# Performance work log

Hardware: AMD Instinct MI355X
Metric: run time of the kernel (lower is better)

Reference implementation:

```python
import jax, jax.numpy as jnp
import numpy as np

# Network dimensions (match init_kwargs)
N_IN, N_HID, N_OUT = 2048, 8192, 1024
N = N_IN + N_HID + N_OUT
BATCH = 512


def setup_inputs() -> dict:
    key = jax.random.key(0)
    k_w, k_b, k_x = jax.random.split(key, 3)
    # GraphNet._init_connections: Xavier-ish std based on (n_inputs + n_outputs)
    std = (2.0 / (N_IN + N_OUT)) ** 0.5
    W = jax.random.normal(k_w, (N, N), dtype=jnp.float32) * std
    # mask: inputs -> hidden, hidden -> outputs (fixed 3-level DAG)
    mask = jnp.zeros((N, N), dtype=jnp.float32)
    mask = mask.at[:N_IN, N_IN:N_IN + N_HID].set(1.0)
    mask = mask.at[N_IN:N_IN + N_HID, N_IN + N_HID:].set(1.0)
    # bias is zero-init in the module; use small random values so it is exercised
    bias = jax.random.normal(k_b, (N,), dtype=jnp.float32) * 0.01
    x = jax.random.normal(k_x, (BATCH, N_IN), dtype=jnp.float32)
    return {"x": x, "W": W, "bias": bias, "mask": mask}


def reference(x, W, bias, mask):
    # Faithful translation of GraphNet.forward for the canonical 3-level
    # topology produced by _init_connections/_compute_levels:
    #   level 0: input nodes [0, N_IN)
    #   level 1: hidden nodes [N_IN, N_IN+N_HID)  -> ReLU
    #   level 2: output nodes [N_IN+N_HID, N)     -> identity (OUTPUT type)
    W_eff = W * mask                       # [N, N] masked adjacency
    B = x.shape[0]
    h = jnp.zeros((B, N), dtype=x.dtype).at[:, :N_IN].set(x)
    # level 1 (hidden): pre_act = h @ W_eff[:, idx] + bias[idx]; ReLU
    pre_h = h @ W_eff[:, N_IN:N_IN + N_HID] + bias[N_IN:N_IN + N_HID]
    h = h.at[:, N_IN:N_IN + N_HID].set(jax.nn.relu(pre_h))
    # level 2 (outputs): pre-activation only (node_type == OUTPUT -> no ReLU)
    pre_o = h @ W_eff[:, N_IN + N_HID:] + bias[N_IN + N_HID:]
    return pre_o                            # h[:, output_indices]
```

## Files before the change

### kernel.cpp

```cpp
#include <hip/hip_runtime.h>

#define N_IN 2048
#define N_HID 8192
#define N_OUT 1024
#define NTOT 11264

typedef __attribute__((ext_vector_type(4))) float f32x4;
typedef __attribute__((ext_vector_type(4))) short short4v;
typedef __attribute__((ext_vector_type(8))) short short8v;
typedef __attribute__((ext_vector_type(2))) unsigned u32x2;

__device__ inline short f2bf(float f) {
    unsigned u = __float_as_uint(f);
    return (short)((u + 0x7fffu + ((u >> 16) & 1u)) >> 16);
}

__device__ inline float bf2f(short s) {
    return __uint_as_float(((unsigned)(unsigned short)s) << 16);
}

__device__ inline unsigned cvt_pk_bf16(float lo, float hi) {
    unsigned r;
    asm("v_cvt_pk_bf16_f32 %0, %1, %2" : "=v"(r) : "v"(lo), "v"(hi));
    return r;
}

__device__ inline int perm64(int c) {
    return (c & 32) + (((c >> 2) & 3) << 3) + (((c >> 4) & 1) << 2) + (c & 3);
}

__device__ inline void gload_lds16(const void* g, void* l) {
    __builtin_amdgcn_global_load_lds(
        (const __attribute__((address_space(1))) unsigned int*)g,
        (__attribute__((address_space(3))) unsigned int*)l, 16, 0, 0);
}

#define WAITV(N) { asm volatile("s_waitcnt vmcnt(" #N ")" ::: "memory"); \
                   __builtin_amdgcn_sched_barrier(0); }
#define BARRIER  { asm volatile("s_waitcnt lgkmcnt(0)" ::: "memory"); \
                   __builtin_amdgcn_sched_barrier(0); \
                   __builtin_amdgcn_s_barrier(); \
                   __builtin_amdgcn_sched_barrier(0); }

__global__ __launch_bounds__(512, 2) void gemm1(
    const float* __restrict__ x,
    const float* __restrict__ W,
    const float* __restrict__ bias,
    short* __restrict__ hOut)
{
    __shared__ __align__(16) short As[2][128 * 64];
    __shared__ __align__(16) short Bs[2][128][72];

    const int bid = blockIdx.x;
    const int xcd = bid & 7;
    const int j   = bid >> 3;
    const int bx  = xcd * 8 + (j >> 2);
    const int by  = j & 3;

    const int t    = threadIdx.x;
    const int lane = t & 63;
    const int wid  = t >> 6;
    const int wr   = wid >> 2;
    const int wc   = wid & 3;
    const int brow = by * 128;
    const int bcol = bx * 128;
    const int l15  = lane & 15;
    const int lg   = lane >> 4;

    const int ar = t >> 2;
    const int kq = (t & 3) * 16;
    const int pbase = ((kq & 32) + ((kq >> 4) & 1) * 4) * 2;
    const int arx = (ar & 7) << 4;
    const float* xrow = x + (size_t)(brow + ar) * N_IN + kq;

    const int nb   = (lane & 7) + 8 * (wid >> 1);
    const int kblk = ((lane >> 3) & 7) + 8 * (wid & 1);
    const int n0 = nb * 4, k0 = kblk * 4;
    const int p0 = perm64(k0);

    f32x4 acc[4][2] = {};
    f32x4 bv0[4], bv1[4], bv2[4];
    f32x4 av0[4], av1[4];

    const float* wp0 = &W[(size_t)k0 * NTOT + (N_IN + bcol + n0)];

#define B_LOAD(TT, BV) { \
    const float* wp = wp0 + (size_t)(TT) * 64 * NTOT; \
    _Pragma("unroll") for (int jj = 0; jj < 4; ++jj) \
        BV[jj] = *reinterpret_cast<const f32x4*>(wp + (size_t)jj * NTOT); }

#define A_LOADR(TT, AV) { \
    const float* xp = xrow + (TT) * 64; \
    _Pragma("unroll") for (int jj = 0; jj < 4; ++jj) \
        AV[jj] = *reinterpret_cast<const f32x4*>(xp + jj * 4); }

#define A_WRITE(TT, AV) { \
    char* dst = (char*)As + ((TT) & 1) * 16384; \
    _Pragma("unroll") for (int jj = 0; jj < 4; ++jj) { \
        u32x2 s; \
        s[0] = cvt_pk_bf16(AV[jj][0], AV[jj][1]); \
        s[1] = cvt_pk_bf16(AV[jj][2], AV[jj][3]); \
        *reinterpret_cast<u32x2*>( \
            dst + ((ar * 128 + pbase + jj * 16) ^ arx)) = s; } }

#define B_WRITE(TT, BV) { \
    short* bsb = &Bs[(TT) & 1][0][0]; \
    _Pragma("unroll") for (int i = 0; i < 4; ++i) { \
        u32x2 s; \
        s[0] = cvt_pk_bf16(BV[0][i], BV[1][i]); \
        s[1] = cvt_pk_bf16(BV[2][i], BV[3][i]); \
        *reinterpret_cast<u32x2*>(bsb + (n0 + i) * 72 + p0) = s; } }

#define COMPUTE(TT) { \
    const char*  ab = (const char*)As + ((TT) & 1) * 16384; \
    const short* bb = &Bs[(TT) & 1][0][0]; \
    short8v a[2][4], b[2][2]; \
    _Pragma("unroll") for (int g = 0; g < 2; ++g) { \
        const int koff = g * 64 + lg * 16; \
        _Pragma("unroll") for (int m = 0; m < 4; ++m) { \
            const int r = wr * 64 + m * 16 + l15; \
            a[g][m] = *reinterpret_cast<const short8v*>( \
                ab + ((r * 128 + koff) ^ ((r & 7) << 4))); } \
        _Pragma("unroll") for (int n = 0; n < 2; ++n) { \
            const int r = wc * 32 + n * 16 + l15; \
            b[g][n] = *reinterpret_cast<const short8v*>( \
                (const char*)(bb + r * 72) + koff); } } \
    __builtin_amdgcn_s_setprio(1); \
    _Pragma("unroll") for (int g = 0; g < 2; ++g) \
      _Pragma("unroll") for (int m = 0; m < 4; ++m) \
        _Pragma("unroll") for (int n = 0; n < 2; ++n) \
            acc[m][n] = __builtin_amdgcn_mfma_f32_16x16x32_bf16( \
                a[g][m], b[g][n], acc[m][n], 0, 0, 0); \
    __builtin_amdgcn_s_setprio(0); }

#define ITER(T, BVL, AVL, AVW, BVW) { \
    B_LOAD(T + 3, BVL); \
    A_LOADR(T + 2, AVL); \
    WAITV(8); \
    A_WRITE(T + 1, AVW); \
    B_WRITE(T + 1, BVW); \
    COMPUTE(T); \
    BARRIER; }

    B_LOAD(0, bv0);
    A_LOADR(0, av0);
    B_LOAD(1, bv1);
    A_LOADR(1, av1);
    B_LOAD(2, bv2);
    WAITV(12);
    A_WRITE(0, av0);
    B_WRITE(0, bv0);
    BARRIER;

    for (int tt = 0; tt < 24; tt += 6) {
        ITER(tt,     bv0, av0, av1, bv1);
        ITER(tt + 1, bv1, av1, av0, bv2);
        ITER(tt + 2, bv2, av0, av1, bv0);
        ITER(tt + 3, bv0, av1, av0, bv1);
        ITER(tt + 4, bv1, av0, av1, bv2);
        ITER(tt + 5, bv2, av1, av0, bv0);
    }
    ITER(24, bv0, av0, av1, bv1);
    ITER(25, bv1, av1, av0, bv2);
    ITER(26, bv2, av0, av1, bv0);
    ITER(27, bv0, av1, av0, bv1);
    ITER(28, bv1, av0, av1, bv2);

    A_LOADR(31, av1);
    WAITV(4);
    A_WRITE(30, av0);
    B_WRITE(30, bv0);
    COMPUTE(29);
    BARRIER;
    WAITV(0);
    A_WRITE(31, av1);
    B_WRITE(31, bv1);
    COMPUTE(30);
    BARRIER;
    COMPUTE(31);

#undef B_LOAD
#undef A_LOADR
#undef A_WRITE
#undef B_WRITE
#undef COMPUTE
#undef ITER

#pragma unroll
    for (int m = 0; m < 4; ++m) {
        const int row0 = brow + wr * 64 + m * 16 + lg * 4;
#pragma unroll
        for (int n = 0; n < 2; ++n) {
            const int col  = bcol + wc * 32 + n * 16 + l15;
            const int pcol = (col & ~63) + perm64(col & 63);
            const float bb = bias[N_IN + col];
#pragma unroll
            for (int q = 0; q < 4; ++q) {
                float v = acc[m][n][q] + bb;
                v = v > 0.f ? v : 0.f;
                hOut[(size_t)(row0 + q) * N_HID + pcol] = f2bf(v);
            }
        }
    }
}

__global__ __launch_bounds__(512, 2) void gemm2(
    const short* __restrict__ A,
    const float* __restrict__ W,
    short* __restrict__ pOut)
{
    __shared__ __align__(16) short As[4][128 * 64];
    __shared__ __align__(16) short Bs[2][128][72];

    const int bid = blockIdx.x;
    const int xcd = bid & 7;
    const int j   = bid >> 3;
    const int xz  = xcd * 8 + (j >> 2);
    const int bx  = xz & 7;
    const int bz  = xz >> 3;
    const int by  = j & 3;

    const int t    = threadIdx.x;
    const int lane = t & 63;
    const int wid  = t >> 6;
    const int wr   = wid >> 2;
    const int wc   = wid & 3;
    const int brow = by * 128;
    const int bcol = bx * 128;
    const int l15  = lane & 15;
    const int lg   = lane >> 4;
    const int ks   = bz * 1024;

    const int arow = lane >> 3;
    const int asw  = ((lane & 7) * 16) ^ (arow << 4);

    const int nb   = (lane & 7) + 8 * (wid >> 1);
    const int kblk = ((lane >> 3) & 7) + 8 * (wid & 1);
    const int n0 = nb * 4, k0 = kblk * 4;
    const int p0 = perm64(k0);

    const char*  Abytes = (const char*)A;
    const size_t lda_b  = (size_t)N_HID * 2;

    f32x4 acc[4][2] = {};
    f32x4 bv0[4], bv1[4], bv2[4], bv3[4];

    const float* wp0 = &W[(size_t)(N_IN + ks + k0) * NTOT
                          + (N_IN + N_HID + bcol + n0)];

#define B_LOAD(TT, BV) { \
    const float* wp = wp0 + (size_t)(TT) * 64 * NTOT; \
    _Pragma("unroll") for (int jj = 0; jj < 4; ++jj) \
        BV[jj] = *reinterpret_cast<const f32x4*>(wp + (size_t)jj * NTOT); }

#define A_LOAD(TT) { \
    char* dst = (char*)As + ((TT) & 3) * 16384; \
    _Pragma("unroll") for (int i = 0; i < 2; ++i) { \
        const int c = wid * 2 + i; \
        gload_lds16(Abytes + (size_t)(brow + c * 8 + arow) * lda_b \
                          + (size_t)(ks + (TT) * 64) * 2 + asw, \
                    dst + c * 1024); } }

#define B_WRITE(TT, BV) { \
    short* bsb = &Bs[(TT) & 1][0][0]; \
    _Pragma("unroll") for (int i = 0; i < 4; ++i) { \
        u32x2 s; \
        s[0] = cvt_pk_bf16(BV[0][i], BV[1][i]); \
        s[1] = cvt_pk_bf16(BV[2][i], BV[3][i]); \
        *reinterpret_cast<u32x2*>(bsb + (n0 + i) * 72 + p0) = s; } }

#define COMPUTE(TT) { \
    const char*  ab = (const char*)As + ((TT) & 3) * 16384; \
    const short* bb = &Bs[(TT) & 1][0][0]; \
    short8v a[2][4], b[2][2]; \
    _Pragma("unroll") for (int g = 0; g < 2; ++g) { \
        const int koff = g * 64 + lg * 16; \
        _Pragma("unroll") for (int m = 0; m < 4; ++m) { \
            const int r = wr * 64 + m * 16 + l15; \
            a[g][m] = *reinterpret_cast<const short8v*>( \
                ab + ((r * 128 + koff) ^ ((r & 7) << 4))); } \
        _Pragma("unroll") for (int n = 0; n < 2; ++n) { \
            const int r = wc * 32 + n * 16 + l15; \
            b[g][n] = *reinterpret_cast<const short8v*>( \
                (const char*)(bb + r * 72) + koff); } } \
    __builtin_amdgcn_s_setprio(1); \
    _Pragma("unroll") for (int g = 0; g < 2; ++g) \
      _Pragma("unroll") for (int m = 0; m < 4; ++m) \
        _Pragma("unroll") for (int n = 0; n < 2; ++n) \
            acc[m][n] = __builtin_amdgcn_mfma_f32_16x16x32_bf16( \
                a[g][m], b[g][n], acc[m][n], 0, 0, 0); \
    __builtin_amdgcn_s_setprio(0); }

#define ITER(T, BVL, BVW) { \
    B_LOAD(T + 3, BVL); A_LOAD(T + 3); \
    WAITV(12); \
    B_WRITE(T + 1, BVW); \
    COMPUTE(T); \
    BARRIER; }

    B_LOAD(0, bv0); A_LOAD(0);
    B_LOAD(1, bv1); A_LOAD(1);
    B_LOAD(2, bv2); A_LOAD(2);
    WAITV(12);
    B_WRITE(0, bv0);
    BARRIER;

    const int nt = 16;
    for (int tt = 0; tt + 4 < nt; tt += 4) {
        ITER(tt,     bv3, bv1);
        ITER(tt + 1, bv0, bv2);
        ITER(tt + 2, bv1, bv3);
        ITER(tt + 3, bv2, bv0);
    }
    ITER(nt - 4, bv3, bv1);

    WAITV(6);
    B_WRITE(nt - 2, bv2);
    COMPUTE(nt - 3);
    BARRIER;
    WAITV(0);
    B_WRITE(nt - 1, bv3);
    COMPUTE(nt - 2);
    BARRIER;
    COMPUTE(nt - 1);

#undef B_LOAD
#undef A_LOAD
#undef B_WRITE
#undef COMPUTE
#undef ITER

    short* po = pOut + (size_t)bz * (512 * N_OUT);
#pragma unroll
    for (int m = 0; m < 4; ++m) {
        const int row0 = brow + wr * 64 + m * 16 + lg * 4;
#pragma unroll
        for (int n = 0; n < 2; ++n) {
            const int col = bcol + wc * 32 + n * 16 + l15;
#pragma unroll
            for (int q = 0; q < 4; ++q)
                po[(size_t)(row0 + q) * N_OUT + col] = f2bf(acc[m][n][q]);
        }
    }
}

__global__ __launch_bounds__(256) void reduce_bias(
    const short* __restrict__ part,
    const float* __restrict__ bias,
    float* __restrict__ out)
{
    const int idx = (blockIdx.x * 256 + threadIdx.x) * 4;
    f32x4 s = *reinterpret_cast<const f32x4*>(&bias[N_IN + N_HID + (idx & 1023)]);
#pragma unroll
    for (int sp = 0; sp < 8; ++sp) {
        const short4v p = *reinterpret_cast<const short4v*>(
            &part[(size_t)sp * 524288 + idx]);
#pragma unroll
        for (int jj = 0; jj < 4; ++jj) s[jj] += bf2f(p[jj]);
    }
    *reinterpret_cast<f32x4*>(&out[idx]) = s;
}

extern "C" void kernel_launch(void* const* d_in, const int* in_sizes, int n_in,
                              void* d_out, int out_size, void* d_ws, size_t ws_size,
                              hipStream_t stream) {
    const float* x    = (const float*)d_in[0];
    const float* W    = (const float*)d_in[1];
    const float* bias = (const float*)d_in[2];
    float* out = (float*)d_out;

    short* h    = (short*)d_ws;
    short* part = (short*)((char*)d_ws + (size_t)(8 << 20));

    gemm1<<<dim3(256), dim3(512), 0, stream>>>(x, W, bias, h);

    gemm2<<<dim3(256), dim3(512), 0, stream>>>(h, W, part);

    reduce_bias<<<dim3(512), dim3(256), 0, stream>>>(part, bias, out);
}
```

Before: 59.32 us.

## Fuse both GEMMs and reduction into one persistent kernel with atomic counters

Merges gemm1, gemm2 and reduce_bias into one kernel of 256 blocks. A block's GEMM2 tile waits on per-tile atomic counters for the GEMM1 tiles it depends on. The last block finishing each output tile does the split-K reduction plus bias. This removes two kernel launch gaps and lets GEMM2 tiles start before all of GEMM1 completes. The cost is a memset launch, spin-waiting on counters, and reliance on all 256 blocks being co-resident to avoid deadlock.

```diff
diff --git a/kernel.cpp b/kernel.cpp
--- a/kernel.cpp
+++ b/kernel.cpp
@@ -14,21 +14,17 @@
     unsigned u = __float_as_uint(f);
     return (short)((u + 0x7fffu + ((u >> 16) & 1u)) >> 16);
 }
-
 __device__ inline float bf2f(short s) {
     return __uint_as_float(((unsigned)(unsigned short)s) << 16);
 }
-
 __device__ inline unsigned cvt_pk_bf16(float lo, float hi) {
     unsigned r;
     asm("v_cvt_pk_bf16_f32 %0, %1, %2" : "=v"(r) : "v"(lo), "v"(hi));
     return r;
 }
-
 __device__ inline int perm64(int c) {
     return (c & 32) + (((c >> 2) & 3) << 3) + (((c >> 4) & 1) << 2) + (c & 3);
 }
-
 __device__ inline void gload_lds16(const void* g, void* l) {
     __builtin_amdgcn_global_load_lds(
         (const __attribute__((address_space(1))) unsigned int*)g,
@@ -42,47 +38,57 @@
                    __builtin_amdgcn_s_barrier(); \
                    __builtin_amdgcn_sched_barrier(0); }
 
-__global__ __launch_bounds__(512, 2) void gemm1(
+__global__ __launch_bounds__(512, 2) void fused_net(
     const float* __restrict__ x,
     const float* __restrict__ W,
     const float* __restrict__ bias,
-    short* __restrict__ hOut)
+    short* __restrict__ h,
+    short* __restrict__ part,
+    float* __restrict__ out,
+    int* __restrict__ cnt)
 {
-    __shared__ __align__(16) short As[2][128 * 64];
-    __shared__ __align__(16) short Bs[2][128][72];
+    __shared__ __align__(16) char smem[102400];
+    __shared__ int isFin;
 
     const int bid = blockIdx.x;
-    const int xcd = bid & 7;
-    const int j   = bid >> 3;
-    const int bx  = xcd * 8 + (j >> 2);
-    const int by  = j & 3;
-
     const int t    = threadIdx.x;
     const int lane = t & 63;
     const int wid  = t >> 6;
     const int wr   = wid >> 2;
     const int wc   = wid & 3;
-    const int brow = by * 128;
-    const int bcol = bx * 128;
     const int l15  = lane & 15;
     const int lg   = lane >> 4;
 
-    const int ar = t >> 2;
-    const int kq = (t & 3) * 16;
-    const int pbase = ((kq & 32) + ((kq >> 4) & 1) * 4) * 2;
-    const int arx = (ar & 7) << 4;
-    const float* xrow = x + (size_t)(brow + ar) * N_IN + kq;
-
-    const int nb   = (lane & 7) + 8 * (wid >> 1);
-    const int kblk = ((lane >> 3) & 7) + 8 * (wid & 1);
-    const int n0 = nb * 4, k0 = kblk * 4;
-    const int p0 = perm64(k0);
-
-    f32x4 acc[4][2] = {};
-    f32x4 bv0[4], bv1[4], bv2[4];
-    f32x4 av0[4], av1[4];
-
-    const float* wp0 = &W[(size_t)k0 * NTOT + (N_IN + bcol + n0)];
+    int* cnt1 = cnt;
+    int* cnt2 = cnt + 32;
+
+    {
+        char*  As1 = smem;
+        short* Bs1 = (short*)(smem + 32768);
+
+        const int xcd = bid & 7;
+        const int j   = bid >> 3;
+        const int bx  = xcd * 8 + (j >> 2);
+        const int by  = j & 3;
+        const int brow = by * 128;
+        const int bcol = bx * 128;
+
+        const int ar = t >> 2;
+        const int kq = (t & 3) * 16;
+        const int pbase = ((kq & 32) + ((kq >> 4) & 1) * 4) * 2;
+        const int arx = (ar & 7) << 4;
+        const float* xrow = x + (size_t)(brow + ar) * N_IN + kq;
+
+        const int nb   = (lane & 7) + 8 * (wid >> 1);
+        const int kblk = ((lane >> 3) & 7) + 8 * (wid & 1);
+        const int n0 = nb * 4, k0 = kblk * 4;
+        const int p0 = perm64(k0);
+
+        f32x4 acc[4][2] = {};
+        f32x4 bv0[4], bv1[4], bv2[4];
+        f32x4 av0[4], av1[4];
+
+        const float* wp0 = &W[(size_t)k0 * NTOT + (N_IN + bcol + n0)];
 
 #define B_LOAD(TT, BV) { \
     const float* wp = wp0 + (size_t)(TT) * 64 * NTOT; \
@@ -95,7 +101,7 @@
         AV[jj] = *reinterpret_cast<const f32x4*>(xp + jj * 4); }
 
 #define A_WRITE(TT, AV) { \
-    char* dst = (char*)As + ((TT) & 1) * 16384; \
+    char* dst = As1 + ((TT) & 1) * 16384; \
     _Pragma("unroll") for (int jj = 0; jj < 4; ++jj) { \
         u32x2 s; \
         s[0] = cvt_pk_bf16(AV[jj][0], AV[jj][1]); \
@@ -104,7 +110,7 @@
             dst + ((ar * 128 + pbase + jj * 16) ^ arx)) = s; } }
 
 #define B_WRITE(TT, BV) { \
-    short* bsb = &Bs[(TT) & 1][0][0]; \
+    short* bsb = Bs1 + ((TT) & 1) * (128 * 72); \
     _Pragma("unroll") for (int i = 0; i < 4; ++i) { \
         u32x2 s; \
         s[0] = cvt_pk_bf16(BV[0][i], BV[1][i]); \
@@ -112,8 +118,8 @@
         *reinterpret_cast<u32x2*>(bsb + (n0 + i) * 72 + p0) = s; } }
 
 #define COMPUTE(TT) { \
-    const char*  ab = (const char*)As + ((TT) & 1) * 16384; \
-    const short* bb = &Bs[(TT) & 1][0][0]; \
+    const char*  ab = As1 + ((TT) & 1) * 16384; \
+    const short* bb = Bs1 + ((TT) & 1) * (128 * 72); \
     short8v a[2][4], b[2][2]; \
     _Pragma("unroll") for (int g = 0; g < 2; ++g) { \
         const int koff = g * 64 + lg * 16; \
@@ -142,42 +148,42 @@
     COMPUTE(T); \
     BARRIER; }
 
-    B_LOAD(0, bv0);
-    A_LOADR(0, av0);
-    B_LOAD(1, bv1);
-    A_LOADR(1, av1);
-    B_LOAD(2, bv2);
-    WAITV(12);
-    A_WRITE(0, av0);
-    B_WRITE(0, bv0);
-    BARRIER;
-
-    for (int tt = 0; tt < 24; tt += 6) {
-        ITER(tt,     bv0, av0, av1, bv1);
-        ITER(tt + 1, bv1, av1, av0, bv2);
-        ITER(tt + 2, bv2, av0, av1, bv0);
-        ITER(tt + 3, bv0, av1, av0, bv1);
-        ITER(tt + 4, bv1, av0, av1, bv2);
-        ITER(tt + 5, bv2, av1, av0, bv0);
-    }
-    ITER(24, bv0, av0, av1, bv1);
-    ITER(25, bv1, av1, av0, bv2);
-    ITER(26, bv2, av0, av1, bv0);
-    ITER(27, bv0, av1, av0, bv1);
-    ITER(28, bv1, av0, av1, bv2);
-
-    A_LOADR(31, av1);
-    WAITV(4);
-    A_WRITE(30, av0);
-    B_WRITE(30, bv0);
-    COMPUTE(29);
-    BARRIER;
-    WAITV(0);
-    A_WRITE(31, av1);
-    B_WRITE(31, bv1);
-    COMPUTE(30);
-    BARRIER;
-    COMPUTE(31);
+        B_LOAD(0, bv0);
+        A_LOADR(0, av0);
+        B_LOAD(1, bv1);
+        A_LOADR(1, av1);
+        B_LOAD(2, bv2);
+        WAITV(12);
+        A_WRITE(0, av0);
+        B_WRITE(0, bv0);
+        BARRIER;
+
+        for (int tt = 0; tt < 24; tt += 6) {
+            ITER(tt,     bv0, av0, av1, bv1);
+            ITER(tt + 1, bv1, av1, av0, bv2);
+            ITER(tt + 2, bv2, av0, av1, bv0);
+            ITER(tt + 3, bv0, av1, av0, bv1);
+            ITER(tt + 4, bv1, av0, av1, bv2);
+            ITER(tt + 5, bv2, av1, av0, bv0);
+        }
+        ITER(24, bv0, av0, av1, bv1);
+        ITER(25, bv1, av1, av0, bv2);
+        ITER(26, bv2, av0, av1, bv0);
+        ITER(27, bv0, av1, av0, bv1);
+        ITER(28, bv1, av0, av1, bv2);
+
+        A_LOADR(31, av1);
+        WAITV(4);
+        A_WRITE(30, av0);
+        B_WRITE(30, bv0);
+        COMPUTE(29);
+        BARRIER;
+        WAITV(0);
+        A_WRITE(31, av1);
+        B_WRITE(31, bv1);
+        COMPUTE(30);
+        BARRIER;
+        COMPUTE(31);
 
 #undef B_LOAD
 #undef A_LOADR
@@ -187,66 +193,73 @@
 #undef ITER
 
 #pragma unroll
-    for (int m = 0; m < 4; ++m) {
-        const int row0 = brow + wr * 64 + m * 16 + lg * 4;
-#pragma unroll
-        for (int n = 0; n < 2; ++n) {
-            const int col  = bcol + wc * 32 + n * 16 + l15;
-            const int pcol = (col & ~63) + perm64(col & 63);
-            const float bb = bias[N_IN + col];
-#pragma unroll
-            for (int q = 0; q < 4; ++q) {
-                float v = acc[m][n][q] + bb;
-                v = v > 0.f ? v : 0.f;
-                hOut[(size_t)(row0 + q) * N_HID + pcol] = f2bf(v);
+        for (int m = 0; m < 4; ++m) {
+            const int row0 = brow + wr * 64 + m * 16 + lg * 4;
+#pragma unroll
+            for (int n = 0; n < 2; ++n) {
+                const int col  = bcol + wc * 32 + n * 16 + l15;
+                const int pcol = (col & ~63) + perm64(col & 63);
+                const float bb = bias[N_IN + col];
+#pragma unroll
+                for (int q = 0; q < 4; ++q) {
+                    float v = acc[m][n][q] + bb;
+                    v = v > 0.f ? v : 0.f;
+                    h[(size_t)(row0 + q) * N_HID + pcol] = f2bf(v);
+                }
             }
         }
+
+        asm volatile("s_waitcnt vmcnt(0)" ::: "memory");
+        __syncthreads();
+        if (t == 0)
+            __hip_atomic_fetch_add(&cnt1[(bx >> 3) * 4 + by], 1,
+                                   __ATOMIC_RELEASE, __HIP_MEMORY_SCOPE_AGENT);
     }
-}
-
-__global__ __launch_bounds__(512, 2) void gemm2(
-    const short* __restrict__ A,
-    const float* __restrict__ W,
-    short* __restrict__ pOut)
-{
-    __shared__ __align__(16) short As[4][128 * 64];
-    __shared__ __align__(16) short Bs[2][128][72];
-
-    const int bid = blockIdx.x;
-    const int xcd = bid & 7;
-    const int j   = bid >> 3;
-    const int xz  = xcd * 8 + (j >> 2);
-    const int bx  = xz & 7;
-    const int bz  = xz >> 3;
-    const int by  = j & 3;
-
-    const int t    = threadIdx.x;
-    const int lane = t & 63;
-    const int wid  = t >> 6;
-    const int wr   = wid >> 2;
-    const int wc   = wid & 3;
-    const int brow = by * 128;
-    const int bcol = bx * 128;
-    const int l15  = lane & 15;
-    const int lg   = lane >> 4;
-    const int ks   = bz * 1024;
-
-    const int arow = lane >> 3;
-    const int asw  = ((lane & 7) * 16) ^ (arow << 4);
-
-    const int nb   = (lane & 7) + 8 * (wid >> 1);
-    const int kblk = ((lane >> 3) & 7) + 8 * (wid & 1);
-    const int n0 = nb * 4, k0 = kblk * 4;
-    const int p0 = perm64(k0);
-
-    const char*  Abytes = (const char*)A;
-    const size_t lda_b  = (size_t)N_HID * 2;
-
-    f32x4 acc[4][2] = {};
-    f32x4 bv0[4], bv1[4], bv2[4], bv3[4];
-
-    const float* wp0 = &W[(size_t)(N_IN + ks + k0) * NTOT
-                          + (N_IN + N_HID + bcol + n0)];
+
+    int fx, fy;
+    {
+        char*  As2 = smem;
+        short* Bs2 = (short*)(smem + 65536);
+
+        const int xcd = bid & 7;
+        const int j   = bid >> 3;
+        const int xz  = xcd * 8 + (j >> 2);
+        const int bx2 = xz & 7;
+        const int bz  = xz >> 3;
+        const int by2 = j & 3;
+        fx = bx2; fy = by2;
+        const int brow = by2 * 128;
+        const int bcol = bx2 * 128;
+        const int ks   = bz * 1024;
+
+        {
+            const int slot = bz * 4 + by2;
+            if (t == 0) {
+                while (__hip_atomic_load(&cnt1[slot], __ATOMIC_RELAXED,
+                                         __HIP_MEMORY_SCOPE_AGENT) < 8)
+                    __builtin_amdgcn_s_sleep(2);
+            }
+            __syncthreads();
+            (void)__hip_atomic_load(&cnt1[slot], __ATOMIC_ACQUIRE,
+                                    __HIP_MEMORY_SCOPE_AGENT);
+            __builtin_amdgcn_sched_barrier(0);
+        }
+
+        const int arow = lane >> 3;
+        const int asw  = ((lane & 7) * 16) ^ (arow << 4);
+        const int nb   = (lane & 7) + 8 * (wid >> 1);
+        const int kblk = ((lane >> 3) & 7) + 8 * (wid & 1);
+        const int n0 = nb * 4, k0 = kblk * 4;
+        const int p0 = perm64(k0);
+
+        const char*  Abytes = (const char*)h;
+        const size_t lda_b  = (size_t)N_HID * 2;
+
+        f32x4 acc[4][2] = {};
+        f32x4 bv0[4], bv1[4], bv2[4], bv3[4];
+
+        const float* wp0 = &W[(size_t)(N_IN + ks + k0) * NTOT
+                              + (N_IN + N_HID + bcol + n0)];
 
 #define B_LOAD(TT, BV) { \
     const float* wp = wp0 + (size_t)(TT) * 64 * NTOT; \
@@ -254,7 +267,7 @@
         BV[jj] = *reinterpret_cast<const f32x4*>(wp + (size_t)jj * NTOT); }
 
 #define A_LOAD(TT) { \
-    char* dst = (char*)As + ((TT) & 3) * 16384; \
+    char* dst = As2 + ((TT) & 3) * 16384; \
     _Pragma("unroll") for (int i = 0; i < 2; ++i) { \
         const int c = wid * 2 + i; \
         gload_lds16(Abytes + (size_t)(brow + c * 8 + arow) * lda_b \
@@ -262,7 +275,7 @@
                     dst + c * 1024); } }
 
 #define B_WRITE(TT, BV) { \
-    short* bsb = &Bs[(TT) & 1][0][0]; \
+    short* bsb = Bs2 + ((TT) & 1) * (128 * 72); \
     _Pragma("unroll") for (int i = 0; i < 4; ++i) { \
         u32x2 s; \
         s[0] = cvt_pk_bf16(BV[0][i], BV[1][i]); \
@@ -270,8 +283,8 @@
         *reinterpret_cast<u32x2*>(bsb + (n0 + i) * 72 + p0) = s; } }
 
 #define COMPUTE(TT) { \
-    const char*  ab = (const char*)As + ((TT) & 3) * 16384; \
-    const short* bb = &Bs[(TT) & 1][0][0]; \
+    const char*  ab = As2 + ((TT) & 3) * 16384; \
+    const short* bb = Bs2 + ((TT) & 1) * (128 * 72); \
     short8v a[2][4], b[2][2]; \
     _Pragma("unroll") for (int g = 0; g < 2; ++g) { \
         const int koff = g * 64 + lg * 16; \
@@ -298,31 +311,31 @@
     COMPUTE(T); \
     BARRIER; }
 
-    B_LOAD(0, bv0); A_LOAD(0);
-    B_LOAD(1, bv1); A_LOAD(1);
-    B_LOAD(2, bv2); A_LOAD(2);
-    WAITV(12);
-    B_WRITE(0, bv0);
-    BARRIER;
-
-    const int nt = 16;
-    for (int tt = 0; tt + 4 < nt; tt += 4) {
-        ITER(tt,     bv3, bv1);
-        ITER(tt + 1, bv0, bv2);
-        ITER(tt + 2, bv1, bv3);
-        ITER(tt + 3, bv2, bv0);
-    }
-    ITER(nt - 4, bv3, bv1);
-
-    WAITV(6);
-    B_WRITE(nt - 2, bv2);
-    COMPUTE(nt - 3);
-    BARRIER;
-    WAITV(0);
-    B_WRITE(nt - 1, bv3);
-    COMPUTE(nt - 2);
-    BARRIER;
-    COMPUTE(nt - 1);
+        B_LOAD(0, bv0); A_LOAD(0);
+        B_LOAD(1, bv1); A_LOAD(1);
+        B_LOAD(2, bv2); A_LOAD(2);
+        WAITV(12);
+        B_WRITE(0, bv0);
+        BARRIER;
+
+        const int nt = 16;
+        for (int tt = 0; tt + 4 < nt; tt += 4) {
+            ITER(tt,     bv3, bv1);
+            ITER(tt + 1, bv0, bv2);
+            ITER(tt + 2, bv1, bv3);
+            ITER(tt + 3, bv2, bv0);
+        }
+        ITER(nt - 4, bv3, bv1);
+
+        WAITV(6);
+        B_WRITE(nt - 2, bv2);
+        COMPUTE(nt - 3);
+        BARRIER;
+        WAITV(0);
+        B_WRITE(nt - 1, bv3);
+        COMPUTE(nt - 2);
+        BARRIER;
+        COMPUTE(nt - 1);
 
 #undef B_LOAD
 #undef A_LOAD
@@ -330,35 +343,56 @@
 #undef COMPUTE
 #undef ITER
 
-    short* po = pOut + (size_t)bz * (512 * N_OUT);
-#pragma unroll
-    for (int m = 0; m < 4; ++m) {
-        const int row0 = brow + wr * 64 + m * 16 + lg * 4;
-#pragma unroll
-        for (int n = 0; n < 2; ++n) {
-            const int col = bcol + wc * 32 + n * 16 + l15;
-#pragma unroll
-            for (int q = 0; q < 4; ++q)
-                po[(size_t)(row0 + q) * N_OUT + col] = f2bf(acc[m][n][q]);
-        }
+        short* po = part + (size_t)bz * (512 * N_OUT);
+#pragma unroll
+        for (int m = 0; m < 4; ++m) {
+            const int row0 = brow + wr * 64 + m * 16 + lg * 4;
+#pragma unroll
+            for (int n = 0; n < 2; ++n) {
+                const int col = bcol + wc * 32 + n * 16 + l15;
+#pragma unroll
+                for (int q = 0; q < 4; ++q)
+                    po[(size_t)(row0 + q) * N_OUT + col] = f2bf(acc[m][n][q]);
+            }
+        }
+
+        asm volatile("s_waitcnt vmcnt(0)" ::: "memory");
+        __syncthreads();
+        if (t == 0) {
+            int old = __hip_atomic_fetch_add(&cnt2[bx2 * 4 + by2], 1,
+                        __ATOMIC_ACQ_REL, __HIP_MEMORY_SCOPE_AGENT);
+            isFin = (old == 7);
+        }
+        __syncthreads();
     }
-}
-
-__global__ __launch_bounds__(256) void reduce_bias(
-    const short* __restrict__ part,
-    const float* __restrict__ bias,
-    float* __restrict__ out)
-{
-    const int idx = (blockIdx.x * 256 + threadIdx.x) * 4;
-    f32x4 s = *reinterpret_cast<const f32x4*>(&bias[N_IN + N_HID + (idx & 1023)]);
-#pragma unroll
-    for (int sp = 0; sp < 8; ++sp) {
-        const short4v p = *reinterpret_cast<const short4v*>(
-            &part[(size_t)sp * 524288 + idx]);
-#pragma unroll
-        for (int jj = 0; jj < 4; ++jj) s[jj] += bf2f(p[jj]);
+
+    if (isFin) {
+        (void)__hip_atomic_load(&cnt2[fx * 4 + fy], __ATOMIC_ACQUIRE,
+                                __HIP_MEMORY_SCOPE_AGENT);
+        __builtin_amdgcn_sched_barrier(0);
+        const int row = t >> 2;
+        const int c0  = (t & 3) * 32;
+        const size_t gr = (size_t)(fy * 128 + row);
+        const int    gc = fx * 128 + c0;
+        f32x4 s[8];
+#pragma unroll
+        for (int jj = 0; jj < 8; ++jj)
+            s[jj] = *reinterpret_cast<const f32x4*>(
+                &bias[N_IN + N_HID + gc + jj * 4]);
+#pragma unroll
+        for (int sp = 0; sp < 8; ++sp) {
+#pragma unroll
+            for (int jj = 0; jj < 8; ++jj) {
+                const short4v p = *reinterpret_cast<const short4v*>(
+                    &part[(size_t)sp * 524288 + gr * 1024 + gc + jj * 4]);
+#pragma unroll
+                for (int e = 0; e < 4; ++e) s[jj][e] += bf2f(p[e]);
+            }
+        }
+#pragma unroll
+        for (int jj = 0; jj < 8; ++jj)
+            *reinterpret_cast<f32x4*>(&out[gr * 1024 + gc + jj * 4]) = s[jj];
     }
-    *reinterpret_cast<f32x4*>(&out[idx]) = s;
 }
 
 extern "C" void kernel_launch(void* const* d_in, const int* in_sizes, int n_in,
@@ -371,10 +405,8 @@
 
     short* h    = (short*)d_ws;
     short* part = (short*)((char*)d_ws + (size_t)(8 << 20));
-
-    gemm1<<<dim3(256), dim3(512), 0, stream>>>(x, W, bias, h);
-
-    gemm2<<<dim3(256), dim3(512), 0, stream>>>(h, W, part);
-
-    reduce_bias<<<dim3(512), dim3(256), 0, stream>>>(part, bias, out);
-}
+    int*   cnt  = (int*)((char*)d_ws + (size_t)(16 << 20));
+
+    hipMemsetAsync(cnt, 0, 64 * sizeof(int), stream);
+    fused_net<<<dim3(256), dim3(512), 0, stream>>>(x, W, bias, h, part, out, cnt);
+}
```

Result: slower. 122.9 us (+107.1%).

## Fuse split-K reduction into gemm2 via last-block atomic counter

Applied to the files above, without the earlier changes.

Removes the separate reduce_bias kernel. Each gemm2 block writes its bf16 split-K partial, then bumps a per-tile atomic counter, and the last of the 8 split blocks for a tile sums all partials plus bias and writes the output. This saves a kernel launch and its tail, but adds a hipMemsetAsync for the counters, serialised reduction work on the final block of each tile, and a fence/atomic cost in every block.

```diff
diff --git a/kernel.cpp b/kernel.cpp
--- a/kernel.cpp
+++ b/kernel.cpp
@@ -14,21 +14,17 @@
     unsigned u = __float_as_uint(f);
     return (short)((u + 0x7fffu + ((u >> 16) & 1u)) >> 16);
 }
-
 __device__ inline float bf2f(short s) {
     return __uint_as_float(((unsigned)(unsigned short)s) << 16);
 }
-
 __device__ inline unsigned cvt_pk_bf16(float lo, float hi) {
     unsigned r;
     asm("v_cvt_pk_bf16_f32 %0, %1, %2" : "=v"(r) : "v"(lo), "v"(hi));
     return r;
 }
-
 __device__ inline int perm64(int c) {
     return (c & 32) + (((c >> 2) & 3) << 3) + (((c >> 4) & 1) << 2) + (c & 3);
 }
-
 __device__ inline void gload_lds16(const void* g, void* l) {
     __builtin_amdgcn_global_load_lds(
         (const __attribute__((address_space(1))) unsigned int*)g,
@@ -207,10 +203,14 @@
 __global__ __launch_bounds__(512, 2) void gemm2(
     const short* __restrict__ A,
     const float* __restrict__ W,
-    short* __restrict__ pOut)
+    const float* __restrict__ bias,
+    short* __restrict__ part,
+    float* __restrict__ out,
+    int* __restrict__ cnt2)
 {
     __shared__ __align__(16) short As[4][128 * 64];
     __shared__ __align__(16) short Bs[2][128][72];
+    __shared__ int isFin;
 
     const int bid = blockIdx.x;
     const int xcd = bid & 7;
@@ -330,7 +330,7 @@
 #undef COMPUTE
 #undef ITER
 
-    short* po = pOut + (size_t)bz * (512 * N_OUT);
+    short* po = part + (size_t)bz * (512 * N_OUT);
 #pragma unroll
     for (int m = 0; m < 4; ++m) {
         const int row0 = brow + wr * 64 + m * 16 + lg * 4;
@@ -342,23 +342,43 @@
                 po[(size_t)(row0 + q) * N_OUT + col] = f2bf(acc[m][n][q]);
         }
     }
-}
-
-__global__ __launch_bounds__(256) void reduce_bias(
-    const short* __restrict__ part,
-    const float* __restrict__ bias,
-    float* __restrict__ out)
-{
-    const int idx = (blockIdx.x * 256 + threadIdx.x) * 4;
-    f32x4 s = *reinterpret_cast<const f32x4*>(&bias[N_IN + N_HID + (idx & 1023)]);
-#pragma unroll
-    for (int sp = 0; sp < 8; ++sp) {
-        const short4v p = *reinterpret_cast<const short4v*>(
-            &part[(size_t)sp * 524288 + idx]);
-#pragma unroll
-        for (int jj = 0; jj < 4; ++jj) s[jj] += bf2f(p[jj]);
-    }
-    *reinterpret_cast<f32x4*>(&out[idx]) = s;
+
+    asm volatile("s_waitcnt vmcnt(0)" ::: "memory");
+    __syncthreads();
+    if (t == 0) {
+        int old = __hip_atomic_fetch_add(&cnt2[bx * 4 + by], 1,
+                    __ATOMIC_ACQ_REL, __HIP_MEMORY_SCOPE_AGENT);
+        isFin = (old == 7);
+    }
+    __syncthreads();
+
+    if (isFin) {
+        (void)__hip_atomic_load(&cnt2[bx * 4 + by], __ATOMIC_ACQUIRE,
+                                __HIP_MEMORY_SCOPE_AGENT);
+        __builtin_amdgcn_sched_barrier(0);
+        const int row = t >> 2;
+        const int c0  = (t & 3) * 32;
+        const size_t gr = (size_t)(by * 128 + row);
+        const int    gc = bx * 128 + c0;
+        f32x4 s[8];
+#pragma unroll
+        for (int jj = 0; jj < 8; ++jj)
+            s[jj] = *reinterpret_cast<const f32x4*>(
+                &bias[N_IN + N_HID + gc + jj * 4]);
+#pragma unroll
+        for (int sp = 0; sp < 8; ++sp) {
+#pragma unroll
+            for (int jj = 0; jj < 8; ++jj) {
+                const short4v p = *reinterpret_cast<const short4v*>(
+                    &part[(size_t)sp * 524288 + gr * 1024 + gc + jj * 4]);
+#pragma unroll
+                for (int e = 0; e < 4; ++e) s[jj][e] += bf2f(p[e]);
+            }
+        }
+#pragma unroll
+        for (int jj = 0; jj < 8; ++jj)
+            *reinterpret_cast<f32x4*>(&out[gr * 1024 + gc + jj * 4]) = s[jj];
+    }
 }
 
 extern "C" void kernel_launch(void* const* d_in, const int* in_sizes, int n_in,
@@ -371,10 +391,10 @@
 
     short* h    = (short*)d_ws;
     short* part = (short*)((char*)d_ws + (size_t)(8 << 20));
+    int*   cnt  = (int*)((char*)d_ws + (size_t)(16 << 20));
+
+    hipMemsetAsync(cnt, 0, 32 * sizeof(int), stream);
 
     gemm1<<<dim3(256), dim3(512), 0, stream>>>(x, W, bias, h);
-
-    gemm2<<<dim3(256), dim3(512), 0, stream>>>(h, W, part);
-
-    reduce_bias<<<dim3(512), dim3(256), 0, stream>>>(part, bias, out);
-}
+    gemm2<<<dim3(256), dim3(512), 0, stream>>>(h, W, bias, part, out, cnt);
+}
```

New measurement: 86.22 us. 1.45x slower.
